# Kernel optimization log

Hardware: AMD Instinct MI355X
Metric: run time of the kernel (lower is better)

## Reference

```python
import jax, jax.numpy as jnp
import numpy as np

B, M, H = 512, 3, 768

def setup_inputs() -> dict:
    key = jax.random.key(0)
    ks = jax.random.split(key, 11)
    s = 1.0 / np.sqrt(H)
    return {
        "target": jax.random.normal(ks[0], (B, H), jnp.float32),
        "cont": jax.random.normal(ks[1], (B, M, H), jnp.float32),
        "Wq": jax.random.uniform(ks[2], (H, H), jnp.float32, -s, s),
        "bq": jax.random.uniform(ks[3], (H,), jnp.float32, -s, s),
        "Wk": jax.random.uniform(ks[4], (H, H), jnp.float32, -s, s),
        "bk": jax.random.uniform(ks[5], (H,), jnp.float32, -s, s),
        "Wv": jax.random.uniform(ks[6], (H, H), jnp.float32, -s, s),
        "bv": jax.random.uniform(ks[7], (H,), jnp.float32, -s, s),
        "p": jax.random.normal(ks[8], (M, H), jnp.float32),
        "h": jax.random.normal(ks[9], (M * H, M), jnp.float32),
        "g": jax.random.normal(ks[10], (M, H), jnp.float32),
    }

def reference(target, cont, Wq, bq, Wk, bk, Wv, bv, p, h, g):
    m = p.shape[0]
    hid = target.shape[-1]
    # torch nn.Linear: y = x @ W.T + b
    query = target @ Wq.T + bq                      # [B, H]
    key_ = cont @ Wk.T + bk                          # [B, m, H]
    value = cont @ Wv.T + bv                         # [B, m, H]
    # kernel_v = p @ query  -> [B, m]
    kernel_v = jnp.einsum('mh,bh->bm', p, query)
    # q = one @ query^T broadcasts query over the m rows, then * key
    x_q = query[:, None, :] * key_                   # [B, m, H]
    kernel_r = x_q.reshape(-1, m * hid) @ h          # [B, m]
    kernel = kernel_v + kernel_r                     # [B, m]
    # _xg = value^T @ g -> [B, H, H]
    _xg = jnp.einsum('bmh,mk->bhk', value, g)        # [B, H, H]
    x_nr = jnp.einsum('bmh,bhk->bmk', value, _xg)    # [B, m, H]
    context = x_nr + value                           # [B, m, H]
    output = jnp.einsum('bm,bmh->bh', kernel, context)  # [B, H]
    return output
```

## Files before the change

kernel.cpp:

```cpp
#include <hip/hip_runtime.h>
#include <hip/hip_bf16.h>

#define HID 768
#define NB  512
#define NM  3

typedef __bf16 bf16x8 __attribute__((ext_vector_type(8)));
typedef float  f32x4  __attribute__((ext_vector_type(4)));

#define WBF_OFF   1572864
#define QKV_OFF   1671168
#define QN        393216
#define KVN       1179648

__device__ __forceinline__ unsigned short f2bf(float f) {
    unsigned u = __builtin_bit_cast(unsigned, f);
    u += 0x7FFFu + ((u >> 16) & 1u);
    return (unsigned short)(u >> 16);
}

__device__ __forceinline__ void async_cp16(const void* g, void* l) {
    __builtin_amdgcn_global_load_lds(
        (const __attribute__((address_space(1))) void*)g,
        (__attribute__((address_space(3))) void*)l, 16, 0, 0);
}

__global__ __launch_bounds__(256) void cvt(
    const float4* __restrict__ t, const float4* __restrict__ c,
    const float4* __restrict__ wq, const float4* __restrict__ wk,
    const float4* __restrict__ wv, ushort4* __restrict__ abf,
    ushort4* __restrict__ wbf)
{
    int i = blockIdx.x * 256 + threadIdx.x;
    float4 v;
    ushort4* d;
    if (i < 393216) {
        v = (i < 98304) ? t[i] : c[i - 98304];
        d = abf + i;
    } else {
        int j = i - 393216;
        v = (j < 147456) ? wq[j] : (j < 294912 ? wk[j - 147456] : wv[j - 294912]);
        d = wbf + j;
    }
    ushort4 o = { f2bf(v.x), f2bf(v.y), f2bf(v.z), f2bf(v.w) };
    *d = o;
}

__global__ __launch_bounds__(256) void qkv_gemm(
    const unsigned short* __restrict__ bfp, float* __restrict__ wsf,
    const float* __restrict__ bq, const float* __restrict__ bk,
    const float* __restrict__ bv)
{
    const unsigned short* Ab = bfp;
    const unsigned short* Wb = bfp + WBF_OFF;
    float* Qf = wsf + QKV_OFF;
    float* Kf = Qf + QN;
    float* Vf = Kf + KVN;

    int t = blockIdx.x;
    const unsigned short *A, *W;
    const float* bias;
    float* C;
    int mtiles;
    if (t < 96)       {          A = Ab;              W = Wb;              bias = bq; C = Qf; mtiles = 8;  }
    else if (t < 384) { t -= 96;  A = Ab + 512 * HID; W = Wb + 768 * HID;  bias = bk; C = Kf; mtiles = 24; }
    else              { t -= 384; A = Ab + 512 * HID; W = Wb + 1536 * HID; bias = bv; C = Vf; mtiles = 24; }
    int tn = t / mtiles, tm = t % mtiles;
    int row0 = tm * 64, col0 = tn * 64;

    __shared__ __align__(16) unsigned short lds[32768];
    char* ldsb = (char*)lds;

    int tid  = threadIdx.x;
    int lane = tid & 63;
    int w    = tid >> 6;
    int q    = lane >> 4;
    int fm   = lane & 15;

    const unsigned short* gA[4];
    const unsigned short* gB[4];
    #pragma unroll
    for (int j = 0; j < 4; j++) {
        int r = j * 16 + w * 4 + q;
        int g = fm ^ (r & 15);
        gA[j] = A + (size_t)(row0 + r) * HID + g * 8;
        gB[j] = W + (size_t)(col0 + r) * HID + g * 8;
    }

    int wm = (w & 1) * 32, wn = (w >> 1) * 32;

    f32x4 acc00 = {0.f, 0.f, 0.f, 0.f};
    f32x4 acc01 = acc00, acc10 = acc00, acc11 = acc00;

    #define STAGE_LOAD(s, kc)                                            \
        {                                                                \
            char* bA_ = ldsb + (s) * 32768;                              \
            char* bB_ = bA_ + 16384;                                     \
            int ko_ = (kc) * 128;                                        \
            _Pragma("unroll")                                            \
            for (int j = 0; j < 4; j++) {                                \
                async_cp16(gA[j] + ko_, bA_ + j * 4096 + w * 1024);      \
                async_cp16(gB[j] + ko_, bB_ + j * 4096 + w * 1024);      \
            }                                                            \
        }

    STAGE_LOAD(0, 0)
    STAGE_LOAD(1, 1)
    __syncthreads();

    #pragma unroll
    for (int c = 0; c < 6; c++) {
        int s = c & 1;
        char* bA = ldsb + s * 32768;
        char* bB = bA + 16384;
        #pragma unroll
        for (int s4 = 0; s4 < 4; s4++) {
            int slot = ((4 * s4 + q) ^ fm) * 16;
            bf16x8 af0 = *(const bf16x8*)(bA + (wm + fm) * 256 + slot);
            bf16x8 af1 = *(const bf16x8*)(bA + (wm + 16 + fm) * 256 + slot);
            bf16x8 bf0 = *(const bf16x8*)(bB + (wn + fm) * 256 + slot);
            bf16x8 bf1 = *(const bf16x8*)(bB + (wn + 16 + fm) * 256 + slot);
            acc00 = __builtin_amdgcn_mfma_f32_16x16x32_bf16(af0, bf0, acc00, 0, 0, 0);
            acc01 = __builtin_amdgcn_mfma_f32_16x16x32_bf16(af0, bf1, acc01, 0, 0, 0);
            acc10 = __builtin_amdgcn_mfma_f32_16x16x32_bf16(af1, bf0, acc10, 0, 0, 0);
            acc11 = __builtin_amdgcn_mfma_f32_16x16x32_bf16(af1, bf1, acc11, 0, 0, 0);
        }
        if (c < 4) {
            __syncthreads();
            STAGE_LOAD(s, c + 2)
        } else if (c == 4) {
            __syncthreads();
        }
    }
    #undef STAGE_LOAD

    int crow = row0 + wm + q * 4;
    int ccol = col0 + wn + fm;
    float bb0 = bias[ccol], bb1 = bias[ccol + 16];
    #pragma unroll
    for (int rg = 0; rg < 4; rg++) {
        C[(size_t)(crow + rg)      * HID + ccol]      = acc00[rg] + bb0;
        C[(size_t)(crow + rg)      * HID + ccol + 16] = acc01[rg] + bb1;
        C[(size_t)(crow + 16 + rg) * HID + ccol]      = acc10[rg] + bb0;
        C[(size_t)(crow + 16 + rg) * HID + ccol + 16] = acc11[rg] + bb1;
    }
}

__global__ __launch_bounds__(256) void finalize(
    const float* __restrict__ wsf, const float* __restrict__ p,
    const float* __restrict__ hmat, const float* __restrict__ g,
    float* __restrict__ out)
{
    int b    = blockIdx.x;
    int tid  = threadIdx.x;
    int lane = tid & 63;
    int wv   = tid >> 6;

    const float* qrow = wsf + QKV_OFF + (size_t)b * HID;
    const float* kk   = wsf + QKV_OFF + QN + (size_t)b * NM * HID;
    const float* vv   = kk + KVN;

    float acc[12];
    #pragma unroll
    for (int i = 0; i < 12; i++) acc[i] = 0.f;

    for (int h0 = tid; h0 < HID; h0 += 256) {
        float qh = qrow[h0];
        float k0 = kk[h0], k1 = kk[HID + h0], k2 = kk[2 * HID + h0];
        float v0 = vv[h0], v1 = vv[HID + h0], v2 = vv[2 * HID + h0];
        acc[0] += p[h0] * qh;
        acc[1] += p[HID + h0] * qh;
        acc[2] += p[2 * HID + h0] * qh;
        float x0 = qh * k0, x1 = qh * k1, x2 = qh * k2;
        const float* h0p = hmat + (size_t)h0 * 3;
        const float* h1p = hmat + (size_t)(HID + h0) * 3;
        const float* h2p = hmat + (size_t)(2 * HID + h0) * 3;
        acc[3] += x0 * h0p[0] + x1 * h1p[0] + x2 * h2p[0];
        acc[4] += x0 * h0p[1] + x1 * h1p[1] + x2 * h2p[1];
        acc[5] += x0 * h0p[2] + x1 * h1p[2] + x2 * h2p[2];
        acc[6]  += v0 * v0; acc[7]  += v0 * v1; acc[8]  += v0 * v2;
        acc[9]  += v1 * v1; acc[10] += v1 * v2; acc[11] += v2 * v2;
    }

    #pragma unroll
    for (int i = 0; i < 12; i++)
        #pragma unroll
        for (int off = 32; off > 0; off >>= 1)
            acc[i] += __shfl_down(acc[i], off);

    __shared__ float sred[12][4];
    __shared__ float fin[12];
    if (lane == 0) {
        #pragma unroll
        for (int i = 0; i < 12; i++) sred[i][wv] = acc[i];
    }
    __syncthreads();
    if (tid < 12) fin[tid] = sred[tid][0] + sred[tid][1] + sred[tid][2] + sred[tid][3];
    __syncthreads();

    float kern0 = fin[0] + fin[3], kern1 = fin[1] + fin[4], kern2 = fin[2] + fin[5];
    float S00 = fin[6], S01 = fin[7], S02 = fin[8];
    float S11 = fin[9], S12 = fin[10], S22 = fin[11];

    for (int cc = tid; cc < HID; cc += 256) {
        float g0 = g[cc], g1 = g[HID + cc], g2 = g[2 * HID + cc];
        float v0 = vv[cc], v1 = vv[HID + cc], v2 = vv[2 * HID + cc];
        float c0 = S00 * g0 + S01 * g1 + S02 * g2 + v0;
        float c1 = S01 * g0 + S11 * g1 + S12 * g2 + v1;
        float c2 = S02 * g0 + S12 * g1 + S22 * g2 + v2;
        out[(size_t)b * HID + cc] = kern0 * c0 + kern1 * c1 + kern2 * c2;
    }
}

extern "C" void kernel_launch(void* const* d_in, const int* in_sizes, int n_in,
                              void* d_out, int out_size, void* d_ws, size_t ws_size,
                              hipStream_t stream) {
    (void)in_sizes; (void)n_in; (void)out_size; (void)ws_size;
    const float* target = (const float*)d_in[0];
    const float* cont   = (const float*)d_in[1];
    const float* Wq     = (const float*)d_in[2];
    const float* bq     = (const float*)d_in[3];
    const float* Wk     = (const float*)d_in[4];
    const float* bk     = (const float*)d_in[5];
    const float* Wv     = (const float*)d_in[6];
    const float* bv     = (const float*)d_in[7];
    const float* p      = (const float*)d_in[8];
    const float* hmat   = (const float*)d_in[9];
    const float* g      = (const float*)d_in[10];

    unsigned short* bfreg = (unsigned short*)d_ws;
    float* wsf = (float*)d_ws;
    float* out = (float*)d_out;

    cvt<<<3264, 256, 0, stream>>>((const float4*)target, (const float4*)cont,
                                  (const float4*)Wq, (const float4*)Wk, (const float4*)Wv,
                                  (ushort4*)bfreg, (ushort4*)(bfreg + WBF_OFF));
    qkv_gemm<<<672, 256, 0, stream>>>(bfreg, wsf, bq, bk, bv);
    finalize<<<512, 256, 0, stream>>>(wsf, p, hmat, g, out);
}
```

Measured before the change: 102.8 us.

## Fuse convert, QKV GEMM and finalize into one cooperative kernel

Merges the three kernels into a single cooperative launch of 512 blocks, using grid-wide syncs between the bf16 conversion, the QKV GEMM and the finalize phases. This removes two kernel launch gaps and the pipeline drain between them. The GEMM now uses a smaller 64-wide K staging (16 KB per stage instead of 32 KB) with a new swizzle, so LDS use drops, which may allow more resident blocks. The cost is that 672 GEMM tiles are spread over 512 blocks, leaving a two-wave imbalance, and two grid barriers are added.

```diff
diff --git a/kernel.cpp b/kernel.cpp
--- a/kernel.cpp
+++ b/kernel.cpp
@@ -1,18 +1,19 @@
 #include <hip/hip_runtime.h>
 #include <hip/hip_bf16.h>
+#include <hip/hip_cooperative_groups.h>
+
+namespace cg = cooperative_groups;
 
 #define HID 768
-#define NB  512
-#define NM  3
-
-typedef __bf16 bf16x8 __attribute__((ext_vector_type(8)));
-typedef float  f32x4  __attribute__((ext_vector_type(4)));
 
 #define WBF_OFF   1572864
 #define QKV_OFF   1671168
 #define QN        393216
 #define KVN       1179648
 
+typedef __bf16 bf16x8 __attribute__((ext_vector_type(8)));
+typedef float  f32x4  __attribute__((ext_vector_type(4)));
+
 __device__ __forceinline__ unsigned short f2bf(float f) {
     unsigned u = __builtin_bit_cast(unsigned, f);
     u += 0x7FFFu + ((u >> 16) & 1u);
@@ -25,190 +26,194 @@
         (__attribute__((address_space(3))) void*)l, 16, 0, 0);
 }
 
-__global__ __launch_bounds__(256) void cvt(
-    const float4* __restrict__ t, const float4* __restrict__ c,
-    const float4* __restrict__ wq, const float4* __restrict__ wk,
-    const float4* __restrict__ wv, ushort4* __restrict__ abf,
-    ushort4* __restrict__ wbf)
+__global__ __launch_bounds__(256) void fused(
+    const float4* __restrict__ t4, const float4* __restrict__ c4,
+    const float4* __restrict__ wq4, const float4* __restrict__ wk4,
+    const float4* __restrict__ wv4,
+    const float* __restrict__ bq, const float* __restrict__ bk,
+    const float* __restrict__ bv,
+    const float* __restrict__ p, const float* __restrict__ hmat,
+    const float* __restrict__ g,
+    float* __restrict__ wsf, float* __restrict__ out)
 {
-    int i = blockIdx.x * 256 + threadIdx.x;
-    float4 v;
-    ushort4* d;
-    if (i < 393216) {
-        v = (i < 98304) ? t[i] : c[i - 98304];
-        d = abf + i;
-    } else {
-        int j = i - 393216;
-        v = (j < 147456) ? wq[j] : (j < 294912 ? wk[j - 147456] : wv[j - 294912]);
-        d = wbf + j;
+    cg::grid_group gg = cg::this_grid();
+    __shared__ __align__(16) char ldsb[32768];
+
+    unsigned short* bfreg = (unsigned short*)wsf;
+    ushort4* abf = (ushort4*)bfreg;
+    ushort4* wbf = (ushort4*)(bfreg + WBF_OFF);
+
+    int tid = threadIdx.x;
+
+    for (int i = blockIdx.x * 256 + tid; i < 835584; i += 512 * 256) {
+        float4 v;
+        ushort4* d;
+        if (i < 393216) {
+            v = (i < 98304) ? t4[i] : c4[i - 98304];
+            d = abf + i;
+        } else {
+            int j = i - 393216;
+            v = (j < 147456) ? wq4[j] : (j < 294912 ? wk4[j - 147456] : wv4[j - 294912]);
+            d = wbf + j;
+        }
+        ushort4 o = { f2bf(v.x), f2bf(v.y), f2bf(v.z), f2bf(v.w) };
+        *d = o;
     }
-    ushort4 o = { f2bf(v.x), f2bf(v.y), f2bf(v.z), f2bf(v.w) };
-    *d = o;
-}
-
-__global__ __launch_bounds__(256) void qkv_gemm(
-    const unsigned short* __restrict__ bfp, float* __restrict__ wsf,
-    const float* __restrict__ bq, const float* __restrict__ bk,
-    const float* __restrict__ bv)
-{
-    const unsigned short* Ab = bfp;
-    const unsigned short* Wb = bfp + WBF_OFF;
+    gg.sync();
+
+    const unsigned short* Ab = bfreg;
+    const unsigned short* Wb = bfreg + WBF_OFF;
     float* Qf = wsf + QKV_OFF;
     float* Kf = Qf + QN;
     float* Vf = Kf + KVN;
 
-    int t = blockIdx.x;
-    const unsigned short *A, *W;
-    const float* bias;
-    float* C;
-    int mtiles;
-    if (t < 96)       {          A = Ab;              W = Wb;              bias = bq; C = Qf; mtiles = 8;  }
-    else if (t < 384) { t -= 96;  A = Ab + 512 * HID; W = Wb + 768 * HID;  bias = bk; C = Kf; mtiles = 24; }
-    else              { t -= 384; A = Ab + 512 * HID; W = Wb + 1536 * HID; bias = bv; C = Vf; mtiles = 24; }
-    int tn = t / mtiles, tm = t % mtiles;
-    int row0 = tm * 64, col0 = tn * 64;
-
-    __shared__ __align__(16) unsigned short lds[32768];
-    char* ldsb = (char*)lds;
-
-    int tid  = threadIdx.x;
-    int lane = tid & 63;
-    int w    = tid >> 6;
-    int q    = lane >> 4;
-    int fm   = lane & 15;
-
-    const unsigned short* gA[4];
-    const unsigned short* gB[4];
-    #pragma unroll
-    for (int j = 0; j < 4; j++) {
-        int r = j * 16 + w * 4 + q;
-        int g = fm ^ (r & 15);
-        gA[j] = A + (size_t)(row0 + r) * HID + g * 8;
-        gB[j] = W + (size_t)(col0 + r) * HID + g * 8;
+    int lane  = tid & 63;
+    int w     = tid >> 6;
+    int q     = lane >> 4;
+    int fm    = lane & 15;
+    int wm    = (w & 1) * 32, wn = (w >> 1) * 32;
+    int srow8 = lane >> 3;
+    int gsw   = (lane & 7) ^ srow8;
+
+    for (int t = blockIdx.x; t < 672; t += 512) {
+        int tt = t;
+        const unsigned short *A, *W;
+        const float* bias;
+        float* C;
+        int mtiles;
+        if (tt < 96)       {           A = Ab;              W = Wb;              bias = bq; C = Qf; mtiles = 8;  }
+        else if (tt < 384) { tt -= 96;  A = Ab + 512 * HID; W = Wb + 768 * HID;  bias = bk; C = Kf; mtiles = 24; }
+        else               { tt -= 384; A = Ab + 512 * HID; W = Wb + 1536 * HID; bias = bv; C = Vf; mtiles = 24; }
+        int tn = tt / mtiles, tm = tt % mtiles;
+        int row0 = tm * 64, col0 = tn * 64;
+
+        const unsigned short* gA[2];
+        const unsigned short* gB[2];
+        #pragma unroll
+        for (int j = 0; j < 2; j++) {
+            int r = j * 32 + w * 8 + srow8;
+            gA[j] = A + (size_t)(row0 + r) * HID + gsw * 8;
+            gB[j] = W + (size_t)(col0 + r) * HID + gsw * 8;
+        }
+
+        f32x4 acc00 = {0.f, 0.f, 0.f, 0.f};
+        f32x4 acc01 = acc00, acc10 = acc00, acc11 = acc00;
+
+        #define STAGE_LOAD(s, kc)                                           \
+            {                                                               \
+                char* bA_ = ldsb + (s) * 16384;                             \
+                char* bB_ = bA_ + 8192;                                     \
+                int ko_ = (kc) * 64;                                        \
+                _Pragma("unroll")                                           \
+                for (int j = 0; j < 2; j++) {                               \
+                    async_cp16(gA[j] + ko_, bA_ + (j * 4 + w) * 1024);      \
+                    async_cp16(gB[j] + ko_, bB_ + (j * 4 + w) * 1024);      \
+                }                                                           \
+            }
+
+        __syncthreads();
+        STAGE_LOAD(0, 0)
+        STAGE_LOAD(1, 1)
+        __syncthreads();
+
+        #pragma unroll
+        for (int c = 0; c < 12; c++) {
+            int s = c & 1;
+            char* bA = ldsb + s * 16384;
+            char* bB = bA + 8192;
+            #pragma unroll
+            for (int s4 = 0; s4 < 2; s4++) {
+                int slot = ((s4 * 4 + q) ^ (fm & 7)) * 16;
+                bf16x8 af0 = *(const bf16x8*)(bA + (wm + fm) * 128 + slot);
+                bf16x8 af1 = *(const bf16x8*)(bA + (wm + 16 + fm) * 128 + slot);
+                bf16x8 bf0 = *(const bf16x8*)(bB + (wn + fm) * 128 + slot);
+                bf16x8 bf1 = *(const bf16x8*)(bB + (wn + 16 + fm) * 128 + slot);
+                acc00 = __builtin_amdgcn_mfma_f32_16x16x32_bf16(af0, bf0, acc00, 0, 0, 0);
+                acc01 = __builtin_amdgcn_mfma_f32_16x16x32_bf16(af0, bf1, acc01, 0, 0, 0);
+                acc10 = __builtin_amdgcn_mfma_f32_16x16x32_bf16(af1, bf0, acc10, 0, 0, 0);
+                acc11 = __builtin_amdgcn_mfma_f32_16x16x32_bf16(af1, bf1, acc11, 0, 0, 0);
+            }
+            if (c < 10) {
+                __syncthreads();
+                STAGE_LOAD(s, c + 2)
+            } else if (c == 10) {
+                __syncthreads();
+            }
+        }
+        #undef STAGE_LOAD
+
+        int crow = row0 + wm + q * 4;
+        int ccol = col0 + wn + fm;
+        float bb0 = bias[ccol], bb1 = bias[ccol + 16];
+        #pragma unroll
+        for (int rg = 0; rg < 4; rg++) {
+            C[(size_t)(crow + rg)      * HID + ccol]      = acc00[rg] + bb0;
+            C[(size_t)(crow + rg)      * HID + ccol + 16] = acc01[rg] + bb1;
+            C[(size_t)(crow + 16 + rg) * HID + ccol]      = acc10[rg] + bb0;
+            C[(size_t)(crow + 16 + rg) * HID + ccol + 16] = acc11[rg] + bb1;
+        }
     }
-
-    int wm = (w & 1) * 32, wn = (w >> 1) * 32;
-
-    f32x4 acc00 = {0.f, 0.f, 0.f, 0.f};
-    f32x4 acc01 = acc00, acc10 = acc00, acc11 = acc00;
-
-    #define STAGE_LOAD(s, kc)                                            \
-        {                                                                \
-            char* bA_ = ldsb + (s) * 32768;                              \
-            char* bB_ = bA_ + 16384;                                     \
-            int ko_ = (kc) * 128;                                        \
-            _Pragma("unroll")                                            \
-            for (int j = 0; j < 4; j++) {                                \
-                async_cp16(gA[j] + ko_, bA_ + j * 4096 + w * 1024);      \
-                async_cp16(gB[j] + ko_, bB_ + j * 4096 + w * 1024);      \
-            }                                                            \
-        }
-
-    STAGE_LOAD(0, 0)
-    STAGE_LOAD(1, 1)
-    __syncthreads();
-
-    #pragma unroll
-    for (int c = 0; c < 6; c++) {
-        int s = c & 1;
-        char* bA = ldsb + s * 32768;
-        char* bB = bA + 16384;
-        #pragma unroll
-        for (int s4 = 0; s4 < 4; s4++) {
-            int slot = ((4 * s4 + q) ^ fm) * 16;
-            bf16x8 af0 = *(const bf16x8*)(bA + (wm + fm) * 256 + slot);
-            bf16x8 af1 = *(const bf16x8*)(bA + (wm + 16 + fm) * 256 + slot);
-            bf16x8 bf0 = *(const bf16x8*)(bB + (wn + fm) * 256 + slot);
-            bf16x8 bf1 = *(const bf16x8*)(bB + (wn + 16 + fm) * 256 + slot);
-            acc00 = __builtin_amdgcn_mfma_f32_16x16x32_bf16(af0, bf0, acc00, 0, 0, 0);
-            acc01 = __builtin_amdgcn_mfma_f32_16x16x32_bf16(af0, bf1, acc01, 0, 0, 0);
-            acc10 = __builtin_amdgcn_mfma_f32_16x16x32_bf16(af1, bf0, acc10, 0, 0, 0);
-            acc11 = __builtin_amdgcn_mfma_f32_16x16x32_bf16(af1, bf1, acc11, 0, 0, 0);
-        }
-        if (c < 4) {
-            __syncthreads();
-            STAGE_LOAD(s, c + 2)
-        } else if (c == 4) {
-            __syncthreads();
-        }
-    }
-    #undef STAGE_LOAD
-
-    int crow = row0 + wm + q * 4;
-    int ccol = col0 + wn + fm;
-    float bb0 = bias[ccol], bb1 = bias[ccol + 16];
-    #pragma unroll
-    for (int rg = 0; rg < 4; rg++) {
-        C[(size_t)(crow + rg)      * HID + ccol]      = acc00[rg] + bb0;
-        C[(size_t)(crow + rg)      * HID + ccol + 16] = acc01[rg] + bb1;
-        C[(size_t)(crow + 16 + rg) * HID + ccol]      = acc10[rg] + bb0;
-        C[(size_t)(crow + 16 + rg) * HID + ccol + 16] = acc11[rg] + bb1;
-    }
-}
-
-__global__ __launch_bounds__(256) void finalize(
-    const float* __restrict__ wsf, const float* __restrict__ p,
-    const float* __restrict__ hmat, const float* __restrict__ g,
-    float* __restrict__ out)
-{
-    int b    = blockIdx.x;
-    int tid  = threadIdx.x;
-    int lane = tid & 63;
-    int wv   = tid >> 6;
-
-    const float* qrow = wsf + QKV_OFF + (size_t)b * HID;
-    const float* kk   = wsf + QKV_OFF + QN + (size_t)b * NM * HID;
-    const float* vv   = kk + KVN;
-
-    float acc[12];
-    #pragma unroll
-    for (int i = 0; i < 12; i++) acc[i] = 0.f;
-
-    for (int h0 = tid; h0 < HID; h0 += 256) {
-        float qh = qrow[h0];
-        float k0 = kk[h0], k1 = kk[HID + h0], k2 = kk[2 * HID + h0];
-        float v0 = vv[h0], v1 = vv[HID + h0], v2 = vv[2 * HID + h0];
-        acc[0] += p[h0] * qh;
-        acc[1] += p[HID + h0] * qh;
-        acc[2] += p[2 * HID + h0] * qh;
-        float x0 = qh * k0, x1 = qh * k1, x2 = qh * k2;
-        const float* h0p = hmat + (size_t)h0 * 3;
-        const float* h1p = hmat + (size_t)(HID + h0) * 3;
-        const float* h2p = hmat + (size_t)(2 * HID + h0) * 3;
-        acc[3] += x0 * h0p[0] + x1 * h1p[0] + x2 * h2p[0];
-        acc[4] += x0 * h0p[1] + x1 * h1p[1] + x2 * h2p[1];
-        acc[5] += x0 * h0p[2] + x1 * h1p[2] + x2 * h2p[2];
-        acc[6]  += v0 * v0; acc[7]  += v0 * v1; acc[8]  += v0 * v2;
-        acc[9]  += v1 * v1; acc[10] += v1 * v2; acc[11] += v2 * v2;
-    }
-
-    #pragma unroll
-    for (int i = 0; i < 12; i++)
-        #pragma unroll
-        for (int off = 32; off > 0; off >>= 1)
-            acc[i] += __shfl_down(acc[i], off);
-
-    __shared__ float sred[12][4];
-    __shared__ float fin[12];
-    if (lane == 0) {
-        #pragma unroll
-        for (int i = 0; i < 12; i++) sred[i][wv] = acc[i];
-    }
-    __syncthreads();
-    if (tid < 12) fin[tid] = sred[tid][0] + sred[tid][1] + sred[tid][2] + sred[tid][3];
-    __syncthreads();
-
-    float kern0 = fin[0] + fin[3], kern1 = fin[1] + fin[4], kern2 = fin[2] + fin[5];
-    float S00 = fin[6], S01 = fin[7], S02 = fin[8];
-    float S11 = fin[9], S12 = fin[10], S22 = fin[11];
-
-    for (int cc = tid; cc < HID; cc += 256) {
-        float g0 = g[cc], g1 = g[HID + cc], g2 = g[2 * HID + cc];
-        float v0 = vv[cc], v1 = vv[HID + cc], v2 = vv[2 * HID + cc];
-        float c0 = S00 * g0 + S01 * g1 + S02 * g2 + v0;
-        float c1 = S01 * g0 + S11 * g1 + S12 * g2 + v1;
-        float c2 = S02 * g0 + S12 * g1 + S22 * g2 + v2;
-        out[(size_t)b * HID + cc] = kern0 * c0 + kern1 * c1 + kern2 * c2;
+    gg.sync();
+
+    {
+        int b    = blockIdx.x;
+        int wv   = tid >> 6;
+        float* sred = (float*)ldsb;
+        float* fin  = (float*)ldsb + 64;
+
+        const float* qrow = wsf + QKV_OFF + (size_t)b * HID;
+        const float* kk   = wsf + QKV_OFF + QN + (size_t)b * 3 * HID;
+        const float* vv   = kk + KVN;
+
+        float acc[12];
+        #pragma unroll
+        for (int i = 0; i < 12; i++) acc[i] = 0.f;
+
+        for (int h0 = tid; h0 < HID; h0 += 256) {
+            float qh = qrow[h0];
+            float k0 = kk[h0], k1 = kk[HID + h0], k2 = kk[2 * HID + h0];
+            float v0 = vv[h0], v1 = vv[HID + h0], v2 = vv[2 * HID + h0];
+            acc[0] += p[h0] * qh;
+            acc[1] += p[HID + h0] * qh;
+            acc[2] += p[2 * HID + h0] * qh;
+            float x0 = qh * k0, x1 = qh * k1, x2 = qh * k2;
+            const float* h0p = hmat + (size_t)h0 * 3;
+            const float* h1p = hmat + (size_t)(HID + h0) * 3;
+            const float* h2p = hmat + (size_t)(2 * HID + h0) * 3;
+            acc[3] += x0 * h0p[0] + x1 * h1p[0] + x2 * h2p[0];
+            acc[4] += x0 * h0p[1] + x1 * h1p[1] + x2 * h2p[1];
+            acc[5] += x0 * h0p[2] + x1 * h1p[2] + x2 * h2p[2];
+            acc[6]  += v0 * v0; acc[7]  += v0 * v1; acc[8]  += v0 * v2;
+            acc[9]  += v1 * v1; acc[10] += v1 * v2; acc[11] += v2 * v2;
+        }
+
+        #pragma unroll
+        for (int i = 0; i < 12; i++)
+            #pragma unroll
+            for (int off = 32; off > 0; off >>= 1)
+                acc[i] += __shfl_down(acc[i], off);
+
+        __syncthreads();
+        if ((tid & 63) == 0) {
+            #pragma unroll
+            for (int i = 0; i < 12; i++) sred[i * 4 + wv] = acc[i];
+        }
+        __syncthreads();
+        if (tid < 12) fin[tid] = sred[tid * 4] + sred[tid * 4 + 1] + sred[tid * 4 + 2] + sred[tid * 4 + 3];
+        __syncthreads();
+
+        float kern0 = fin[0] + fin[3], kern1 = fin[1] + fin[4], kern2 = fin[2] + fin[5];
+        float S00 = fin[6], S01 = fin[7], S02 = fin[8];
+        float S11 = fin[9], S12 = fin[10], S22 = fin[11];
+
+        for (int cc = tid; cc < HID; cc += 256) {
+            float g0 = g[cc], g1 = g[HID + cc], g2 = g[2 * HID + cc];
+            float v0 = vv[cc], v1 = vv[HID + cc], v2 = vv[2 * HID + cc];
+            float c0 = S00 * g0 + S01 * g1 + S02 * g2 + v0;
+            float c1 = S01 * g0 + S11 * g1 + S12 * g2 + v1;
+            float c2 = S02 * g0 + S12 * g1 + S22 * g2 + v2;
+            out[(size_t)b * HID + cc] = kern0 * c0 + kern1 * c1 + kern2 * c2;
+        }
     }
 }
 
@@ -216,25 +221,22 @@
                               void* d_out, int out_size, void* d_ws, size_t ws_size,
                               hipStream_t stream) {
     (void)in_sizes; (void)n_in; (void)out_size; (void)ws_size;
-    const float* target = (const float*)d_in[0];
-    const float* cont   = (const float*)d_in[1];
-    const float* Wq     = (const float*)d_in[2];
-    const float* bq     = (const float*)d_in[3];
-    const float* Wk     = (const float*)d_in[4];
-    const float* bk     = (const float*)d_in[5];
-    const float* Wv     = (const float*)d_in[6];
-    const float* bv     = (const float*)d_in[7];
-    const float* p      = (const float*)d_in[8];
-    const float* hmat   = (const float*)d_in[9];
-    const float* g      = (const float*)d_in[10];
-
-    unsigned short* bfreg = (unsigned short*)d_ws;
+    const float4* t4  = (const float4*)d_in[0];
+    const float4* c4  = (const float4*)d_in[1];
+    const float4* wq4 = (const float4*)d_in[2];
+    const float*  bq  = (const float*)d_in[3];
+    const float4* wk4 = (const float4*)d_in[4];
+    const float*  bk  = (const float*)d_in[5];
+    const float4* wv4 = (const float4*)d_in[6];
+    const float*  bv  = (const float*)d_in[7];
+    const float*  p   = (const float*)d_in[8];
+    const float*  hm  = (const float*)d_in[9];
+    const float*  g   = (const float*)d_in[10];
     float* wsf = (float*)d_ws;
     float* out = (float*)d_out;
 
-    cvt<<<3264, 256, 0, stream>>>((const float4*)target, (const float4*)cont,
-                                  (const float4*)Wq, (const float4*)Wk, (const float4*)Wv,
-                                  (ushort4*)bfreg, (ushort4*)(bfreg + WBF_OFF));
-    qkv_gemm<<<672, 256, 0, stream>>>(bfreg, wsf, bq, bk, bv);
-    finalize<<<512, 256, 0, stream>>>(wsf, p, hmat, g, out);
-}
+    void* args[13] = { &t4, &c4, &wq4, &wk4, &wv4, &bq, &bk, &bv,
+                       &p, &hm, &g, &wsf, &out };
+    hipLaunchCooperativeKernel((const void*)fused, dim3(512), dim3(256),
+                               args, 0, stream);
+}
```

Result: slower. 243.6 us (+137.0%).
